# Optimization experiments

Hardware: AMD Instinct MI355X
Metric: run time of the kernel (lower is better)

The kernel has to match this reference:

```python
import jax, jax.numpy as jnp
import numpy as np

T, B, HW, C_IN, NA, HID = 64, 64, 42, 4, 12, 256
FEAT = 288  # 32 channels * 3 * 3 spatial after 4 stride-2 convs


def setup_inputs() -> dict:
    key = jax.random.key(0)
    ks = jax.random.split(key, 16)
    g = lambda k, s, sc=0.1: jax.random.normal(k, s, jnp.float32) * sc
    z = lambda s: jnp.zeros(s, jnp.float32)
    return {
        "frame": jax.random.uniform(ks[0], (T, B, HW, HW, C_IN), jnp.float32),
        "done": jax.random.bernoulli(ks[1], 0.05, (T, B)),
        "h0": z((2, B, HID)),
        "c0": z((2, B, HID)),
        "conv_w1": g(ks[2], (32, C_IN, 3, 3)), "conv_b1": z((32,)),
        "conv_w2": g(ks[3], (32, 32, 3, 3)), "conv_b2": z((32,)),
        "conv_w3": g(ks[4], (32, 32, 3, 3)), "conv_b3": z((32,)),
        "conv_w4": g(ks[5], (32, 32, 3, 3)), "conv_b4": z((32,)),
        "w_ih0": g(ks[6], (4 * HID, FEAT)), "w_hh0": g(ks[7], (4 * HID, HID)),
        "b_ih0": z((4 * HID,)), "b_hh0": z((4 * HID,)),
        "w_ih1": g(ks[8], (4 * HID, HID)), "w_hh1": g(ks[9], (4 * HID, HID)),
        "b_ih1": z((4 * HID,)), "b_hh1": z((4 * HID,)),
        "policy_w": g(ks[10], (NA, HID)), "policy_b": z((NA,)),
        "baseline_w": g(ks[11], (1, HID)), "baseline_b": z((1,)),
    }


def _lstm_step(x, h, c, w_ih, w_hh, b_ih, b_hh):
    # PyTorch LSTM gate order: i, f, g, o
    gates = x @ w_ih.T + h @ w_hh.T + b_ih + b_hh
    i, f, g, o = jnp.split(gates, 4, axis=-1)
    c_new = jax.nn.sigmoid(f) * c + jax.nn.sigmoid(i) * jnp.tanh(g)
    h_new = jax.nn.sigmoid(o) * jnp.tanh(c_new)
    return h_new, c_new


def reference(frame, done, h0, c0,
              conv_w1, conv_b1, conv_w2, conv_b2, conv_w3, conv_b3, conv_w4, conv_b4,
              w_ih0, w_hh0, b_ih0, b_hh0, w_ih1, w_hh1, b_ih1, b_hh1,
              policy_w, policy_b, baseline_w, baseline_b):
    T_, B_ = frame.shape[:2]
    # torch: view(T,B,W,H,C) [relabel only] -> flatten -> transpose(1,3) == permute(0,3,2,1)
    x = frame.reshape(T_ * B_, HW, HW, C_IN).transpose(0, 3, 2, 1)  # [TB, C, H, W]
    for w, b in ((conv_w1, conv_b1), (conv_w2, conv_b2), (conv_w3, conv_b3), (conv_w4, conv_b4)):
        x = jax.lax.conv_general_dilated(x, w, (2, 2), ((1, 1), (1, 1)),
                                         dimension_numbers=("NCHW", "OIHW", "NCHW"))
        x = jax.nn.elu(x + b[None, :, None, None])
    core_input = x.reshape(T_, B_, FEAT)
    notdone = (~done).astype(jnp.float32)  # [T, B]

    def step(carry, xs):
        h, c = carry           # [2, B, HID] each
        x_t, nd = xs           # [B, FEAT], [B]
        m = nd[None, :, None]
        h, c = h * m, c * m    # reset state where episode ended
        h0n, c0n = _lstm_step(x_t, h[0], c[0], w_ih0, w_hh0, b_ih0, b_hh0)
        h1n, c1n = _lstm_step(h0n, h[1], c[1], w_ih1, w_hh1, b_ih1, b_hh1)
        return (jnp.stack([h0n, h1n]), jnp.stack([c0n, c1n])), h1n

    (hT, cT), outs = jax.lax.scan(step, (h0, c0), (core_input, notdone))
    core_output = outs.reshape(T_ * B_, HID)
    policy_logits = core_output @ policy_w.T + policy_b
    baseline = core_output @ baseline_w.T + baseline_b
    action = jnp.argmax(policy_logits, axis=1)  # eval-mode action
    return (policy_logits.reshape(T_, B_, NA), baseline.reshape(T_, B_),
            action.reshape(T_, B_), hT, cT)
```

## Files before the change

kernel.cpp:

```cpp
#include <hip/hip_runtime.h>
#include <hip/hip_bf16.h>


#define T_ 64
#define B_ 64
#define NTB 4096
#define HID 256
#define G4 1024

typedef float f4 __attribute__((ext_vector_type(4)));

#define XS(j) ((((j) << 2)) ^ ((((j) >> 3) & 7) << 2))

__device__ inline float sigm(float x) { return 1.f / (1.f + __expf(-x)); }
__device__ inline float tanh_(float x) { return 1.f - 2.f / (1.f + __expf(2.f * x)); }
__device__ inline float elu_(float x) { return x > 0.f ? x : __expf(x) - 1.f; }

__global__ void k_prep(const float* __restrict__ wih0, const float* __restrict__ wih1,
                       const float* __restrict__ whh0, const float* __restrict__ whh1,
                       const float* __restrict__ cw2, const float* __restrict__ cw3,
                       const float* __restrict__ cw4, const float* __restrict__ pw,
                       const float* __restrict__ bw,
                       float* __restrict__ wih0T, float* __restrict__ wih1T,
                       float* __restrict__ wq0, float* __restrict__ wq1,
                       float* __restrict__ wc2, float* __restrict__ wc3,
                       float* __restrict__ wc4, float* __restrict__ pwT) {
  int idx = blockIdx.x * 256 + threadIdx.x;
  if (idx < 294912) {
    int k = idx >> 10, j = idx & 1023;
    wih0T[idx] = wih0[j * 288 + k];
  } else if (idx < 557056) {
    int r = idx - 294912; int k = r >> 10, j = r & 1023;
    wih1T[r] = wih1[j * 256 + k];
  } else if (idx < 819200) {
    int r = idx - 557056;
    int cc = r & 3, row = (r >> 2) & 1023, k4 = r >> 12;
    wq0[r] = whh0[row * 256 + k4 * 4 + cc];
  } else if (idx < 1081344) {
    int r = idx - 819200;
    int cc = r & 3, row = (r >> 2) & 1023, k4 = r >> 12;
    wq1[r] = whh1[row * 256 + k4 * 4 + cc];
  } else if (idx < 1108992) {
    int r = idx - 1081344;
    int which = r / 9216; int d = r - which * 9216;
    int i = d & 31, tap = (d >> 5) % 9, o = d / 288;
    int kh = tap / 3, kw = tap - kh * 3;
    const float* src = which == 0 ? cw2 : (which == 1 ? cw3 : cw4);
    float* dst = which == 0 ? wc2 : (which == 1 ? wc3 : wc4);
    dst[d] = src[((o * 32 + i) * 3 + kh) * 3 + kw];
  } else if (idx < 1113088) {
    int r = idx - 1108992; int k = r >> 4, o = r & 15;
    pwT[r] = o < 12 ? pw[o * 256 + k] : (o == 12 ? bw[k] : 0.f);
  }
}

__global__ __launch_bounds__(1024)
void k_donecvt(const unsigned char* __restrict__ db, float* __restrict__ nd) {
  int tid = threadIdx.x;
  const unsigned* dw = (const unsigned*)db;
  unsigned w = dw[tid];
  int odd = ((w & 0xFFFFFF00u) != 0u && w != 0x3F800000u) ? 1 : 0;
  int any = __syncthreads_count(odd);
  bool u8 = (any > 0);
  for (int j = tid; j < 4096; j += 1024) {
    unsigned v = u8 ? (unsigned)db[j] : dw[j];
    nd[j] = v ? 0.f : 1.f;
  }
}

__global__ __launch_bounds__(512, 8)
void k_convall(const float* __restrict__ frame, const float* __restrict__ cw1,
               const float* __restrict__ cb1, const float* __restrict__ wc2,
               const float* __restrict__ cb2, const float* __restrict__ wc3,
               const float* __restrict__ cb3, const float* __restrict__ wc4,
               const float* __restrict__ cb4, float* __restrict__ featT) {
  __shared__ __align__(16) float a1t[8][1792];
  __shared__ __align__(16) float act2l[8][512];
  __shared__ __align__(16) float act3l[8][192];
  int n = blockIdx.x;
  int tid = threadIdx.x;
  const float4* fp = (const float4*)(frame + (size_t)n * 7056);

  if (tid < 441) {
    int p = tid / 21, q = tid - (tid / 21) * 21;
    float px[9][4];
#pragma unroll
    for (int kh = 0; kh < 3; ++kh) {
#pragma unroll
      for (int kw = 0; kw < 3; ++kw) {
        int A = 2 * p - 1 + kh, Bc = 2 * q - 1 + kw;
        bool ok = ((unsigned)A < 42u) && ((unsigned)Bc < 42u);
        float4 v = ok ? fp[Bc * 42 + A] : make_float4(0.f, 0.f, 0.f, 0.f);
        px[kh * 3 + kw][0] = v.x; px[kh * 3 + kw][1] = v.y;
        px[kh * 3 + kw][2] = v.z; px[kh * 3 + kw][3] = v.w;
      }
    }
    int col = XS(tid);
#pragma unroll
    for (int oq = 0; oq < 8; ++oq) {
      float4 acc;
      float* ap = (float*)&acc;
#pragma unroll
      for (int j = 0; j < 4; ++j) {
        int o = oq * 4 + j;
        float a = cb1[o];
        const float* w = cw1 + o * 36;
#pragma unroll
        for (int tap = 0; tap < 9; ++tap)
          a += px[tap][0] * w[tap] + px[tap][1] * w[9 + tap] +
               px[tap][2] * w[18 + tap] + px[tap][3] * w[27 + tap];
        ap[j] = elu_(a);
      }
      *(float4*)&a1t[oq][col] = acc;
    }
  }
  __syncthreads();

  {
    int s = tid & 127, oh = tid >> 7;
    int ob = __builtin_amdgcn_readfirstlane(oh << 3);
    if (s < 121) {
      int p = s / 11, q = s - (s / 11) * 11;
      float acc[8];
#pragma unroll
      for (int oi = 0; oi < 8; ++oi) acc[oi] = cb2[ob + oi];
#pragma unroll
      for (int kh = 0; kh < 3; ++kh) {
        int A = 2 * p - 1 + kh;
        if ((unsigned)A >= 21u) continue;
#pragma unroll
        for (int kw = 0; kw < 3; ++kw) {
          int Bc = 2 * q - 1 + kw;
          if ((unsigned)Bc >= 21u) continue;
          int pos = A * 21 + Bc;
          int col = XS(pos);
          int tap = kh * 3 + kw;
#pragma unroll
          for (int i4 = 0; i4 < 8; ++i4) {
            float4 v = *(const float4*)&a1t[i4][col];
#pragma unroll
            for (int oi = 0; oi < 8; ++oi) {
              const float* w = wc2 + ((ob + oi) * 9 + tap) * 32 + i4 * 4;
              acc[oi] += v.x * w[0] + v.y * w[1] + v.z * w[2] + v.w * w[3];
            }
          }
        }
      }
      int colw = XS(s);
#pragma unroll
      for (int half = 0; half < 2; ++half) {
        float4 o4 = make_float4(elu_(acc[half * 4 + 0]), elu_(acc[half * 4 + 1]),
                                elu_(acc[half * 4 + 2]), elu_(acc[half * 4 + 3]));
        *(float4*)&act2l[(ob >> 2) + half][colw] = o4;
      }
    }
  }
  __syncthreads();

  {
    int wv = tid >> 6, lane = tid & 63;
    int oq = __builtin_amdgcn_readfirstlane(wv);
    if (lane < 36) {
      int p = lane / 6, q = lane - (lane / 6) * 6;
      float acc[4];
#pragma unroll
      for (int j = 0; j < 4; ++j) acc[j] = cb3[oq * 4 + j];
#pragma unroll
      for (int kh = 0; kh < 3; ++kh) {
        int A = 2 * p - 1 + kh;
        if ((unsigned)A >= 11u) continue;
#pragma unroll
        for (int kw = 0; kw < 3; ++kw) {
          int Bc = 2 * q - 1 + kw;
          if ((unsigned)Bc >= 11u) continue;
          int col = XS(A * 11 + Bc);
          int tap = kh * 3 + kw;
#pragma unroll
          for (int i4 = 0; i4 < 8; ++i4) {
            float4 v = *(const float4*)&act2l[i4][col];
#pragma unroll
            for (int j = 0; j < 4; ++j) {
              const float* w = wc3 + ((oq * 4 + j) * 9 + tap) * 32 + i4 * 4;
              acc[j] += v.x * w[0] + v.y * w[1] + v.z * w[2] + v.w * w[3];
            }
          }
        }
      }
      float4 o4 = make_float4(elu_(acc[0]), elu_(acc[1]), elu_(acc[2]), elu_(acc[3]));
      *(float4*)&act3l[oq][XS(p * 6 + q)] = o4;
    }
  }
  __syncthreads();

  {
    int wv = tid >> 6, lane = tid & 63;
    int oq = __builtin_amdgcn_readfirstlane(wv);
    if (lane < 9) {
      int p = lane / 3, q = lane - (lane / 3) * 3;
      float acc[4];
#pragma unroll
      for (int j = 0; j < 4; ++j) acc[j] = cb4[oq * 4 + j];
#pragma unroll
      for (int kh = 0; kh < 3; ++kh) {
        int A = 2 * p - 1 + kh;
        if ((unsigned)A >= 6u) continue;
#pragma unroll
        for (int kw = 0; kw < 3; ++kw) {
          int Bc = 2 * q - 1 + kw;
          if ((unsigned)Bc >= 6u) continue;
          int col = XS(A * 6 + Bc);
          int tap = kh * 3 + kw;
#pragma unroll
          for (int i4 = 0; i4 < 8; ++i4) {
            float4 v = *(const float4*)&act3l[i4][col];
#pragma unroll
            for (int j = 0; j < 4; ++j) {
              const float* w = wc4 + ((oq * 4 + j) * 9 + tap) * 32 + i4 * 4;
              acc[j] += v.x * w[0] + v.y * w[1] + v.z * w[2] + v.w * w[3];
            }
          }
        }
      }
#pragma unroll
      for (int j = 0; j < 4; ++j)
        featT[(size_t)((oq * 4 + j) * 9 + lane) * 4096 + n] = elu_(acc[j]);
    }
  }
}

__global__ __launch_bounds__(256)
void k_gemm2(const float* __restrict__ inT, const float* __restrict__ wT,
             const float* __restrict__ b1, const float* __restrict__ b2,
             float* __restrict__ out, int K) {
  int nb = blockIdx.x >> 4, jb = blockIdx.x & 15;
  int lane = threadIdx.x & 63, wv = threadIdx.x >> 6;
  int n = nb * 64 + lane;
  int j0 = jb * 64 + __builtin_amdgcn_readfirstlane(wv << 4);
  float acc[16];
#pragma unroll
  for (int m = 0; m < 16; ++m) acc[m] = 0.f;
  const float* ip = inT + n;
#pragma unroll 4
  for (int k = 0; k < K; ++k) {
    float x = ip[(size_t)k * 4096];
    const float* w = wT + k * 1024 + j0;
#pragma unroll
    for (int m = 0; m < 16; ++m) acc[m] += x * w[m];
  }
  float* op = out + (size_t)n * 1024 + j0;
#pragma unroll
  for (int h = 0; h < 4; ++h) {
    float4 o4 = make_float4(acc[h * 4 + 0] + b1[j0 + h * 4 + 0] + b2[j0 + h * 4 + 0],
                            acc[h * 4 + 1] + b1[j0 + h * 4 + 1] + b2[j0 + h * 4 + 1],
                            acc[h * 4 + 2] + b1[j0 + h * 4 + 2] + b2[j0 + h * 4 + 2],
                            acc[h * 4 + 3] + b1[j0 + h * 4 + 3] + b2[j0 + h * 4 + 3]);
    *(float4*)&op[h * 4] = o4;
  }
}

#define WREGS(X) X(0) X(1) X(2) X(3) X(4) X(5) X(6) X(7) \
                 X(8) X(9) X(10) X(11) X(12) X(13) X(14) X(15)

__global__ __launch_bounds__(1024, 4)
void k_scan(const float* __restrict__ wq, const float* __restrict__ G,
            const float* __restrict__ h_init, const float* __restrict__ c_init,
            const float* __restrict__ ndb, float* __restrict__ h_allT,
            float* __restrict__ hT, float* __restrict__ cT) {
  int b = blockIdx.x, j = threadIdx.x;
  __shared__ __align__(16) float hs[256];
  __shared__ __align__(16) f4 wl[9][1024];
  __shared__ float gl[1024];
  const f4* wq4 = (const f4*)wq;
#define DECLR(i) f4 wr##i = wq4[(i) * 1024 + j];
  WREGS(DECLR)
#undef DECLR
#pragma unroll
  for (int q = 0; q < 9; ++q) wl[q][j] = wq4[(16 + q) * 1024 + j];
  float c = 0.f;
  if (j < 256) { hs[j] = h_init[b * HID + j]; c = c_init[b * HID + j]; }
  __syncthreads();
  const f4* hs4 = (const f4*)hs;
  const f4* sp = wq4 + 25 * 1024 + j;
  const float* gp = G + b * G4 + j;
  float hlast = 0.f;
  for (int t = 0; t < T_; ++t) {
    float nd = ndb[t * B_ + b];
    f4 acc = {0.f, 0.f, 0.f, 0.f};
#define FMAR(i) { f4 h4 = hs4[i]; acc += h4 * wr##i; }
    WREGS(FMAR)
#undef FMAR
#pragma unroll
    for (int q = 0; q < 9; ++q) { f4 h4 = hs4[16 + q]; acc += h4 * wl[q][j]; }
#pragma unroll 4
    for (int q = 0; q < 39; ++q) { f4 h4 = hs4[25 + q]; acc += h4 * sp[(size_t)q * 1024]; }
    float g = gp[(size_t)t * (B_ * G4)] + (acc.x + acc.y + acc.z + acc.w) * nd;
    gl[j] = g;
    __syncthreads();
    if (j < 256) {
      float gi = gl[j], gf = gl[j + 256], gg = gl[j + 512], go = gl[j + 768];
      c = sigm(gf) * (c * nd) + sigm(gi) * tanh_(gg);
      float h = sigm(go) * tanh_(c);
      hs[j] = h;
      h_allT[(size_t)j * 4096 + t * B_ + b] = h;
      hlast = h;
    }
    __syncthreads();
  }
  if (j < 256) { hT[b * HID + j] = hlast; cT[b * HID + j] = c; }
}

__global__ __launch_bounds__(256)
void k_heads(const float* __restrict__ h1aT, const float* __restrict__ pwT,
             const float* __restrict__ pb, const float* __restrict__ bb,
             float* __restrict__ out) {
  int n = blockIdx.x * 256 + threadIdx.x;
  float acc[13];
#pragma unroll
  for (int o = 0; o < 12; ++o) acc[o] = pb[o];
  acc[12] = bb[0];
  for (int k = 0; k < 256; ++k) {
    float h = h1aT[(size_t)k * 4096 + n];
    const float* w = pwT + k * 16;
#pragma unroll
    for (int o = 0; o < 13; ++o) acc[o] += h * w[o];
  }
  float best = acc[0]; int bi = 0;
#pragma unroll
  for (int o = 1; o < 12; ++o)
    if (acc[o] > best) { best = acc[o]; bi = o; }
#pragma unroll
  for (int o = 0; o < 12; ++o) out[n * 12 + o] = acc[o];
  out[49152 + n] = acc[12];
  out[53248 + n] = (float)bi;
}

extern "C" void kernel_launch(void* const* d_in, const int* in_sizes, int n_in,
                              void* d_out, int out_size, void* d_ws, size_t ws_size,
                              hipStream_t stream) {
  const float* frame = (const float*)d_in[0];
  const unsigned char* done = (const unsigned char*)d_in[1];
  const float* h0 = (const float*)d_in[2];
  const float* c0 = (const float*)d_in[3];
  const float* cw1 = (const float*)d_in[4];  const float* cb1 = (const float*)d_in[5];
  const float* cw2 = (const float*)d_in[6];  const float* cb2 = (const float*)d_in[7];
  const float* cw3 = (const float*)d_in[8];  const float* cb3 = (const float*)d_in[9];
  const float* cw4 = (const float*)d_in[10]; const float* cb4 = (const float*)d_in[11];
  const float* wih0 = (const float*)d_in[12]; const float* whh0 = (const float*)d_in[13];
  const float* bih0 = (const float*)d_in[14]; const float* bhh0 = (const float*)d_in[15];
  const float* wih1 = (const float*)d_in[16]; const float* whh1 = (const float*)d_in[17];
  const float* bih1 = (const float*)d_in[18]; const float* bhh1 = (const float*)d_in[19];
  const float* pw = (const float*)d_in[20]; const float* pb = (const float*)d_in[21];
  const float* bw = (const float*)d_in[22]; const float* bb = (const float*)d_in[23];

  float* featT = (float*)d_ws;
  float* G0    = featT + 1179648;
  float* G1    = G0 + 4194304;
  float* h0aT  = G1 + 4194304;
  float* h1aT  = h0aT + 1048576;
  float* wih0T = h1aT + 1048576;
  float* wih1T = wih0T + 294912;
  float* wq0   = wih1T + 262144;
  float* wq1   = wq0 + 262144;
  float* wc2   = wq1 + 262144;
  float* wc3   = wc2 + 9216;
  float* wc4   = wc3 + 9216;
  float* pwT   = wc4 + 9216;
  float* ndb   = pwT + 4096;

  float* out = (float*)d_out;
  float* o_hT = out + 57344;
  float* o_cT = out + 90112;

  k_prep<<<4348, 256, 0, stream>>>(wih0, wih1, whh0, whh1, cw2, cw3, cw4, pw, bw,
                                   wih0T, wih1T, wq0, wq1, wc2, wc3, wc4, pwT);
  k_donecvt<<<1, 1024, 0, stream>>>(done, ndb);
  k_convall<<<4096, 512, 0, stream>>>(frame, cw1, cb1, wc2, cb2, wc3, cb3, wc4, cb4,
                                      featT);
  k_gemm2<<<1024, 256, 0, stream>>>(featT, wih0T, bih0, bhh0, G0, 288);
  k_scan<<<64, 1024, 0, stream>>>(wq0, G0, h0, c0, ndb, h0aT, o_hT, o_cT);
  k_gemm2<<<1024, 256, 0, stream>>>(h0aT, wih1T, bih1, bhh1, G1, 256);
  k_scan<<<64, 1024, 0, stream>>>(wq1, G1, h0 + 16384, c0 + 16384, ndb, h1aT,
                                  o_hT + 16384, o_cT + 16384);
  k_heads<<<16, 256, 0, stream>>>(h1aT, pwT, pb, bb, out);
}
```

Before: 1.707 ms.

## Split conv1 output channels into two halves to shrink conv1 LDS buffer

Conv1 now computes its 32 output channels in two passes of 16. Conv2 accumulates partial sums over each half of its input channels between passes, so the a1t shared buffer halves in size. The aim is to cut LDS per block and raise occupancy. The cost is reloading the frame pixels twice, an extra barrier per pass, and conv2 accumulators held live across both passes; launch bounds drop from 8 to 6 waves.

Measured after the change: 2.049 ms. +20.1%, slower.

```diff
diff --git a/kernel.cpp b/kernel.cpp
--- a/kernel.cpp
+++ b/kernel.cpp
@@ -68,62 +68,64 @@
   }
 }
 
-__global__ __launch_bounds__(512, 8)
+__global__ __launch_bounds__(512, 6)
 void k_convall(const float* __restrict__ frame, const float* __restrict__ cw1,
                const float* __restrict__ cb1, const float* __restrict__ wc2,
                const float* __restrict__ cb2, const float* __restrict__ wc3,
                const float* __restrict__ cb3, const float* __restrict__ wc4,
                const float* __restrict__ cb4, float* __restrict__ featT) {
-  __shared__ __align__(16) float a1t[8][1792];
+  __shared__ __align__(16) float a1t[4][1792];
   __shared__ __align__(16) float act2l[8][512];
   __shared__ __align__(16) float act3l[8][192];
   int n = blockIdx.x;
   int tid = threadIdx.x;
   const float4* fp = (const float4*)(frame + (size_t)n * 7056);
 
-  if (tid < 441) {
-    int p = tid / 21, q = tid - (tid / 21) * 21;
-    float px[9][4];
-#pragma unroll
-    for (int kh = 0; kh < 3; ++kh) {
-#pragma unroll
-      for (int kw = 0; kw < 3; ++kw) {
-        int A = 2 * p - 1 + kh, Bc = 2 * q - 1 + kw;
-        bool ok = ((unsigned)A < 42u) && ((unsigned)Bc < 42u);
-        float4 v = ok ? fp[Bc * 42 + A] : make_float4(0.f, 0.f, 0.f, 0.f);
-        px[kh * 3 + kw][0] = v.x; px[kh * 3 + kw][1] = v.y;
-        px[kh * 3 + kw][2] = v.z; px[kh * 3 + kw][3] = v.w;
-      }
-    }
-    int col = XS(tid);
-#pragma unroll
-    for (int oq = 0; oq < 8; ++oq) {
-      float4 acc;
-      float* ap = (float*)&acc;
-#pragma unroll
-      for (int j = 0; j < 4; ++j) {
-        int o = oq * 4 + j;
-        float a = cb1[o];
-        const float* w = cw1 + o * 36;
-#pragma unroll
-        for (int tap = 0; tap < 9; ++tap)
-          a += px[tap][0] * w[tap] + px[tap][1] * w[9 + tap] +
-               px[tap][2] * w[18 + tap] + px[tap][3] * w[27 + tap];
-        ap[j] = elu_(a);
-      }
-      *(float4*)&a1t[oq][col] = acc;
-    }
-  }
-  __syncthreads();
-
-  {
-    int s = tid & 127, oh = tid >> 7;
-    int ob = __builtin_amdgcn_readfirstlane(oh << 3);
-    if (s < 121) {
-      int p = s / 11, q = s - (s / 11) * 11;
-      float acc[8];
-#pragma unroll
-      for (int oi = 0; oi < 8; ++oi) acc[oi] = cb2[ob + oi];
+  int sC = tid & 127, ohC = tid >> 7;
+  int obC = __builtin_amdgcn_readfirstlane(ohC << 3);
+  float acc2[8];
+#pragma unroll
+  for (int oi = 0; oi < 8; ++oi) acc2[oi] = cb2[obC + oi];
+
+#pragma unroll
+  for (int h = 0; h < 2; ++h) {
+    if (tid < 441) {
+      int p = tid / 21, q = tid - (tid / 21) * 21;
+      float accb[4][4];
+#pragma unroll
+      for (int oq = 0; oq < 4; ++oq)
+#pragma unroll
+        for (int j = 0; j < 4; ++j) accb[oq][j] = cb1[(h * 4 + oq) * 4 + j];
+#pragma unroll
+      for (int kh = 0; kh < 3; ++kh) {
+#pragma unroll
+        for (int kw = 0; kw < 3; ++kw) {
+          int A = 2 * p - 1 + kh, Bc = 2 * q - 1 + kw;
+          bool ok = ((unsigned)A < 42u) && ((unsigned)Bc < 42u);
+          float4 v = ok ? fp[Bc * 42 + A] : make_float4(0.f, 0.f, 0.f, 0.f);
+          int tap = kh * 3 + kw;
+#pragma unroll
+          for (int oq = 0; oq < 4; ++oq)
+#pragma unroll
+            for (int j = 0; j < 4; ++j) {
+              const float* w = cw1 + ((h * 4 + oq) * 4 + j) * 36;
+              accb[oq][j] += v.x * w[tap] + v.y * w[9 + tap] +
+                             v.z * w[18 + tap] + v.w * w[27 + tap];
+            }
+        }
+      }
+      int col = XS(tid);
+#pragma unroll
+      for (int oq = 0; oq < 4; ++oq) {
+        float4 o4 = make_float4(elu_(accb[oq][0]), elu_(accb[oq][1]),
+                                elu_(accb[oq][2]), elu_(accb[oq][3]));
+        *(float4*)&a1t[oq][col] = o4;
+      }
+    }
+    __syncthreads();
+
+    if (sC < 121) {
+      int p = sC / 11, q = sC - (sC / 11) * 11;
 #pragma unroll
       for (int kh = 0; kh < 3; ++kh) {
         int A = 2 * p - 1 + kh;
@@ -132,27 +134,30 @@
         for (int kw = 0; kw < 3; ++kw) {
           int Bc = 2 * q - 1 + kw;
           if ((unsigned)Bc >= 21u) continue;
-          int pos = A * 21 + Bc;
-          int col = XS(pos);
+          int col = XS(A * 21 + Bc);
           int tap = kh * 3 + kw;
 #pragma unroll
-          for (int i4 = 0; i4 < 8; ++i4) {
+          for (int i4 = 0; i4 < 4; ++i4) {
             float4 v = *(const float4*)&a1t[i4][col];
 #pragma unroll
             for (int oi = 0; oi < 8; ++oi) {
-              const float* w = wc2 + ((ob + oi) * 9 + tap) * 32 + i4 * 4;
-              acc[oi] += v.x * w[0] + v.y * w[1] + v.z * w[2] + v.w * w[3];
+              const float* w = wc2 + ((obC + oi) * 9 + tap) * 32 + (h * 4 + i4) * 4;
+              acc2[oi] += v.x * w[0] + v.y * w[1] + v.z * w[2] + v.w * w[3];
             }
           }
         }
       }
-      int colw = XS(s);
-#pragma unroll
-      for (int half = 0; half < 2; ++half) {
-        float4 o4 = make_float4(elu_(acc[half * 4 + 0]), elu_(acc[half * 4 + 1]),
-                                elu_(acc[half * 4 + 2]), elu_(acc[half * 4 + 3]));
-        *(float4*)&act2l[(ob >> 2) + half][colw] = o4;
-      }
+    }
+    __syncthreads();
+  }
+
+  if (sC < 121) {
+    int colw = XS(sC);
+#pragma unroll
+    for (int half = 0; half < 2; ++half) {
+      float4 o4 = make_float4(elu_(acc2[half * 4 + 0]), elu_(acc2[half * 4 + 1]),
+                              elu_(acc2[half * 4 + 2]), elu_(acc2[half * 4 + 3]));
+      *(float4*)&act2l[(obC >> 2) + half][colw] = o4;
     }
   }
   __syncthreads();
```
